# Kernel tuning notes

Measured on AMD Instinct MI355X. Metric: run time of the kernel, lower is better.

Reference implementation:

```python
import jax, jax.numpy as jnp
import numpy as np

VOCAB, HID, KS, VS, EMB = 30, 512, 128, 128, 256
T, N, MAXLEN = 1000, 256, 250

def _lstm_cell(x, h, c, w_ih, w_hh, b_ih, b_hh):
    gates = x @ w_ih.T + h @ w_hh.T + b_ih + b_hh
    i, f, g, o = jnp.split(gates, 4, axis=-1)
    c2 = jax.nn.sigmoid(f) * c + jax.nn.sigmoid(i) * jnp.tanh(g)
    h2 = jax.nn.sigmoid(o) * jnp.tanh(c2)
    return h2, c2

def setup_inputs() -> dict:
    key = jax.random.key(0)
    ks = jax.random.split(key, 20)
    p = lambda k, shp: (jax.random.normal(k, shp, dtype=jnp.float32) * 0.05)
    inp = {
        'keys': jax.random.normal(ks[0], (T, N, KS), dtype=jnp.float32),
        'values': jax.random.normal(ks[1], (T, N, VS), dtype=jnp.float32),
        'seq_lengths': jax.random.randint(ks[2], (N,), 1, T + 1),
        'text': jax.random.randint(ks[3], (N, MAXLEN), 0, VOCAB),
        'embed_W': p(ks[4], (VOCAB, EMB)),
        'w_ih1': p(ks[5], (4 * HID, EMB + VS)), 'w_hh1': p(ks[6], (4 * HID, HID)),
        'b_ih1': jnp.zeros((4 * HID,), jnp.float32), 'b_hh1': jnp.zeros((4 * HID,), jnp.float32),
        'w_ih2': p(ks[7], (4 * HID, HID)), 'w_hh2': p(ks[8], (4 * HID, HID)),
        'b_ih2': jnp.zeros((4 * HID,), jnp.float32), 'b_hh2': jnp.zeros((4 * HID,), jnp.float32),
        'w_ih3': p(ks[9], (4 * KS, HID)), 'w_hh3': p(ks[10], (4 * KS, KS)),
        'b_ih3': jnp.zeros((4 * KS,), jnp.float32), 'b_hh3': jnp.zeros((4 * KS,), jnp.float32),
        'lin_W': p(ks[11], (KS, KS + VS)), 'lin_b': jnp.zeros((KS,), jnp.float32),
        'char_W': p(ks[12], (VOCAB, KS)), 'char_b': jnp.zeros((VOCAB,), jnp.float32),
    }
    return inp

def reference(keys, values, seq_lengths, text, embed_W,
              w_ih1, w_hh1, b_ih1, b_hh1,
              w_ih2, w_hh2, b_ih2, b_hh2,
              w_ih3, w_hh3, b_ih3, b_hh3,
              lin_W, lin_b, char_W, char_b):
    # teacher forcing path (deterministic), dropout is identity in reference
    mask = jnp.arange(T)[None, :] >= seq_lengths[:, None]          # (N, T)
    embs = embed_W[text]                                           # (N, MAXLEN, EMB)
    embs = jnp.swapaxes(embs, 0, 1)                                # (MAXLEN, N, EMB)

    def step(carry, emb_t):
        h1, c1, h2, c2, h3, c3, ctx = carry
        inp1 = jnp.concatenate([emb_t, ctx], axis=1)
        h1, c1 = _lstm_cell(inp1, h1, c1, w_ih1, w_hh1, b_ih1, b_hh1)
        h2, c2 = _lstm_cell(h1, h2, c2, w_ih2, w_hh2, b_ih2, b_hh2)
        h3, c3 = _lstm_cell(h2, h3, c3, w_ih3, w_hh3, b_ih3, b_hh3)
        energy = jnp.einsum('tnk,nk->nt', keys, h3)                # (N, T)
        energy = jnp.where(mask, -1e9, energy)
        attn = jax.nn.softmax(energy, axis=1)
        ctx2 = jnp.einsum('nt,tnv->nv', attn, values)              # (N, VS)
        pred = jnp.concatenate([h3, ctx2], axis=1) @ lin_W.T + lin_b
        pred = pred @ char_W.T + char_b                            # (N, VOCAB)
        return (h1, c1, h2, c2, h3, c3, ctx2), (pred, attn)

    z = lambda d: jnp.zeros((N, d), jnp.float32)
    init = (z(HID), z(HID), z(HID), z(HID), z(KS), z(KS), values[-1])
    _, (preds, attns) = jax.lax.scan(step, init, embs)
    return jnp.swapaxes(preds, 0, 1), attns                        # (N, MAXLEN, VOCAB), (MAXLEN, N, T)
```

## Files before the change

kernel.cpp:

```cpp
#include <hip/hip_runtime.h>

#define VOCAB  30
#define HID    512
#define KS     128
#define VS     128
#define EMB    256
#define TT     1000
#define NB     256
#define MAXLEN 250

#define NH (NB*HID)
#define NK (NB*KS)
#define OFF_CTX (6*NH + 3*NK)
#define WS_TOTAL (OFF_CTX + NK)
#define STATE_BYTES ((size_t)WS_TOTAL * 4)
#define VBF_BYTES   ((size_t)TT * NB * VS * 2)

#define K1 (EMB + VS + HID)
#define K2 (HID + HID)
#define K3 (HID + KS)
#define W1SZ (4*HID*K1)
#define W2SZ (4*HID*K2)
#define W3SZ (4*KS*K3)
#define EMBSZ (VOCAB*EMB)
#define BS1 (4*HID)
#define BS2 (4*HID)
#define BS3 (4*KS)

constexpr size_t NEW_BASE  = STATE_BYTES + VBF_BYTES;
constexpr size_t OFF_W1HI  = NEW_BASE;
constexpr size_t OFF_W1LO  = OFF_W1HI + (size_t)W1SZ*2;
constexpr size_t OFF_W2HI  = OFF_W1LO + (size_t)W1SZ*2;
constexpr size_t OFF_W2LO  = OFF_W2HI + (size_t)W2SZ*2;
constexpr size_t OFF_W3HI  = OFF_W2LO + (size_t)W2SZ*2;
constexpr size_t OFF_W3LO  = OFF_W3HI + (size_t)W3SZ*2;
constexpr size_t OFF_EMBHI = OFF_W3LO + (size_t)W3SZ*2;
constexpr size_t OFF_EMBLO = OFF_EMBHI + (size_t)EMBSZ*2;
constexpr size_t OFF_BSUM  = OFF_EMBLO + (size_t)EMBSZ*2;
constexpr size_t OFF_CTXHI = OFF_BSUM  + (size_t)(BS1+BS2+BS3)*4;
constexpr size_t OFF_CTXLO = OFF_CTXHI + (size_t)NB*VS*2;
constexpr size_t OFF_H1HI  = OFF_CTXLO + (size_t)NB*VS*2;
constexpr size_t OFF_H1LO  = OFF_H1HI + (size_t)2*NH*2;
constexpr size_t OFF_H2HI  = OFF_H1LO + (size_t)2*NH*2;
constexpr size_t OFF_H2LO  = OFF_H2HI + (size_t)2*NH*2;
constexpr size_t OFF_H3HI  = OFF_H2LO + (size_t)2*NH*2;
constexpr size_t OFF_H3LO  = OFF_H3HI + (size_t)2*NK*2;
constexpr size_t OFF_H3F   = OFF_H3LO + (size_t)2*NK*2;
constexpr size_t OFF_C1    = OFF_H3F  + (size_t)NK*4;
constexpr size_t OFF_C2    = OFF_C1 + (size_t)NH*4;
constexpr size_t OFF_C3    = OFF_C2 + (size_t)NH*4;
constexpr size_t FULL_BYTES= OFF_C3 + (size_t)NK*4;
constexpr size_t ZERO_BASE = OFF_H1HI;
constexpr size_t ZERO_BYTES= FULL_BYTES - OFF_H1HI;

typedef __attribute__((ext_vector_type(8))) short bf16x8;
typedef __attribute__((ext_vector_type(4))) float f32x4;
typedef unsigned short u16;

__device__ __forceinline__ float sigmoidf_(float x){ return 1.0f/(1.0f+__expf(-x)); }

__device__ __forceinline__ u16 f2bf_(float x){
    unsigned int u = __float_as_uint(x);
    return (u16)((u + 0x7fffu + ((u >> 16) & 1u)) >> 16);
}
__device__ __forceinline__ float bf2f_(u16 h){ return __uint_as_float((unsigned)h << 16); }


__global__ __launch_bounds__(256)
void pack_w_kernel(const float* __restrict__ wih, const float* __restrict__ whh,
                   u16* __restrict__ hi, u16* __restrict__ lo, int KIN, int KH, int total)
{
    int i = blockIdx.x*256 + threadIdx.x;
    if (i >= total) return;
    const int KW = KIN + KH;
    int g = i / KW, k = i - g*KW;
    float v = (k < KIN) ? wih[g*KIN + k] : whh[g*KH + (k - KIN)];
    u16 h = f2bf_(v);
    hi[i] = h;
    lo[i] = f2bf_(v - bf2f_(h));
}

__global__ __launch_bounds__(256)
void prep_misc_kernel(char* __restrict__ wsb, const float* __restrict__ embW,
                      const float* __restrict__ bi1, const float* __restrict__ bh1,
                      const float* __restrict__ bi2, const float* __restrict__ bh2,
                      const float* __restrict__ bi3, const float* __restrict__ bh3,
                      const float* __restrict__ values)
{
    const int gt = blockIdx.x*256 + threadIdx.x;
    const int gs = gridDim.x*256;
    u16* Ehi = (u16*)(wsb + OFF_EMBHI);
    u16* Elo = (u16*)(wsb + OFF_EMBLO);
    for (int i = gt; i < EMBSZ; i += gs){
        float v = embW[i]; u16 h = f2bf_(v);
        Ehi[i]=h; Elo[i]=f2bf_(v - bf2f_(h));
    }
    float* bs = (float*)(wsb + OFF_BSUM);
    for (int i = gt; i < BS1; i += gs) bs[i]         = bi1[i]+bh1[i];
    for (int i = gt; i < BS2; i += gs) bs[BS1+i]     = bi2[i]+bh2[i];
    for (int i = gt; i < BS3; i += gs) bs[BS1+BS2+i] = bi3[i]+bh3[i];
    u16* Chi = (u16*)(wsb + OFF_CTXHI);
    u16* Clo = (u16*)(wsb + OFF_CTXLO);
    const float* v0 = values + (size_t)(TT-1)*NB*VS;
    for (int i = gt; i < NB*VS; i += gs){
        float v = v0[i]; u16 h = f2bf_(v);
        Chi[i]=h; Clo[i]=f2bf_(v - bf2f_(h));
    }
    uint4* z = (uint4*)(wsb + ZERO_BASE);
    uint4 zz; zz.x=0; zz.y=0; zz.z=0; zz.w=0;
    for (size_t i = (size_t)gt; i < ZERO_BYTES/16; i += (size_t)gs) z[i] = zz;
}


__device__ __forceinline__ void lstm_step(const u16* const wh[4], const u16* const wl[4], int kw,
                                          bf16x8 ah, bf16x8 al, f32x4 acc[4])
{
    #pragma unroll
    for (int q=0;q<4;q++){
        bf16x8 wH = *(const bf16x8*)(wh[q] + kw);
        bf16x8 wL = *(const bf16x8*)(wl[q] + kw);
        acc[q] = __builtin_amdgcn_mfma_f32_16x16x32_bf16(ah, wH, acc[q], 0,0,0);
        acc[q] = __builtin_amdgcn_mfma_f32_16x16x32_bf16(al, wH, acc[q], 0,0,0);
        acc[q] = __builtin_amdgcn_mfma_f32_16x16x32_bf16(ah, wL, acc[q], 0,0,0);
    }
}

template<int H, int KIN, int KH, int MODE>
__global__ __launch_bounds__(128)
void lstm_mfma(const u16* __restrict__ Whi, const u16* __restrict__ Wlo,
               const float* __restrict__ bsum,
               const u16* __restrict__ xhi, const u16* __restrict__ xlo,
               const u16* __restrict__ ehi, const u16* __restrict__ elo,
               const int* __restrict__ text, int step,
               const u16* __restrict__ hphi, const u16* __restrict__ hplo,
               u16* __restrict__ hohi, u16* __restrict__ holo,
               float* __restrict__ hof,
               float* __restrict__ cbuf)
{
    constexpr int KW = KIN + KH;
    constexpr int HT = H/16;
    const int lane = threadIdx.x & 63;
    const int gw   = blockIdx.x*2 + (threadIdx.x >> 6);
    const int ht   = gw % HT, nt = gw / HT;
    const int l15  = lane & 15, lhi = lane >> 4;
    const int n    = nt*16 + l15;
    const int koff = lhi*8;
    const int h0   = ht*16;

    const u16* wh[4]; const u16* wl[4];
    #pragma unroll
    for (int q=0;q<4;q++){
        size_t off = (size_t)(q*H + h0 + l15)*KW + koff;
        wh[q] = Whi + off; wl[q] = Wlo + off;
    }

    f32x4 acc[4];
    f32x4 zr = {0.f,0.f,0.f,0.f};
    #pragma unroll
    for (int q=0;q<4;q++) acc[q] = zr;

    int kb;
    if constexpr (MODE == 0) {
        const int trow = text[n*MAXLEN + step];
        const u16* Eh = ehi + trow*EMB + koff;
        const u16* El = elo + trow*EMB + koff;
        #pragma unroll 4
        for (int s=0;s<EMB/32;s++)
            lstm_step(wh, wl, s*32, *(const bf16x8*)(Eh + s*32), *(const bf16x8*)(El + s*32), acc);
        const u16* Ch = xhi + n*VS + koff;
        const u16* Cl = xlo + n*VS + koff;
        #pragma unroll
        for (int s=0;s<VS/32;s++)
            lstm_step(wh, wl, EMB + s*32, *(const bf16x8*)(Ch + s*32), *(const bf16x8*)(Cl + s*32), acc);
        kb = EMB + VS;
    } else {
        const u16* Xh = xhi + n*KIN + koff;
        const u16* Xl = xlo + n*KIN + koff;
        #pragma unroll 4
        for (int s=0;s<KIN/32;s++)
            lstm_step(wh, wl, s*32, *(const bf16x8*)(Xh + s*32), *(const bf16x8*)(Xl + s*32), acc);
        kb = KIN;
    }
    {
        const u16* Hh = hphi + n*KH + koff;
        const u16* Hl = hplo + n*KH + koff;
        #pragma unroll 4
        for (int s=0;s<KH/32;s++)
            lstm_step(wh, wl, kb + s*32, *(const bf16x8*)(Hh + s*32), *(const bf16x8*)(Hl + s*32), acc);
    }

    const int hcol = h0 + l15;
    const float b0 = bsum[0*H + hcol], b1 = bsum[1*H + hcol];
    const float b2 = bsum[2*H + hcol], b3 = bsum[3*H + hcol];
    const int nr0 = nt*16 + lhi*4;
    #pragma unroll
    for (int r=0;r<4;r++){
        const size_t p = (size_t)(nr0 + r)*H + hcol;
        const float gi = acc[0][r] + b0;
        const float gf = acc[1][r] + b1;
        const float gg = acc[2][r] + b2;
        const float go = acc[3][r] + b3;
        const float cn = sigmoidf_(gf)*cbuf[p] + sigmoidf_(gi)*tanhf(gg);
        const float hn = sigmoidf_(go)*tanhf(cn);
        cbuf[p] = cn;
        const u16 hb = f2bf_(hn);
        hohi[p] = hb;
        holo[p] = f2bf_(hn - bf2f_(hb));
        if (hof) hof[p] = hn;
    }
}


__global__ __launch_bounds__(256)
void init_kernel(float* __restrict__ ws, const float* __restrict__ values){
    int i = blockIdx.x*256 + threadIdx.x;
    if (i >= WS_TOTAL) return;
    if (i < OFF_CTX) ws[i] = 0.0f;
    else ws[i] = values[(size_t)(TT-1)*NB*VS + (i - OFF_CTX)];
}

__global__ __launch_bounds__(256)
void conv_bf16_kernel(const float* __restrict__ src, u16* __restrict__ dst, int n4){
    int i = blockIdx.x*256 + threadIdx.x;
    if (i >= n4) return;
    float4 v = ((const float4*)src)[i];
    ushort4 o;
    o.x = f2bf_(v.x); o.y = f2bf_(v.y); o.z = f2bf_(v.z); o.w = f2bf_(v.w);
    ((ushort4*)dst)[i] = o;
}

template<int H, int KX, int KH, int MODE>
__global__ __launch_bounds__(256)
void lstm_kernel(const float* __restrict__ Wx, const float* __restrict__ Wh,
                 const float* __restrict__ bx, const float* __restrict__ bh,
                 const float* __restrict__ xbuf, const float* __restrict__ embW,
                 const int* __restrict__ text, int step,
                 const float* __restrict__ hread, float* __restrict__ hwrite,
                 float* __restrict__ cbuf)
{
    __shared__ __align__(16) float Xs[16][68];
    __shared__ __align__(16) float Ws[16][68];
    __shared__ float Gs[64][65];

    const int tid = threadIdx.x;
    const int h0  = blockIdx.x * 16;
    const int n0  = blockIdx.y * 64;

    const int sr = tid >> 2;
    const int sk = (tid & 3) << 2;
    const int wrow = (sr >> 4) * H + h0 + (sr & 15);
    const int n  = n0 + sr;

    const int tn4 = (tid & 15) * 4;
    const int tc4 = (tid >> 4) * 4;

    float acc[4][4];
    #pragma unroll
    for (int i=0;i<4;i++){
        #pragma unroll
        for (int j=0;j<4;j++) acc[i][j]=0.0f;
    }

    for (int k0 = 0; k0 < KX + KH; k0 += 16) {
        const int kb = k0 + sk;
        float4 xv, wv;
        if (k0 < KX) {
            if constexpr (MODE == 0) {
                if (kb < EMB) {
                    int idx = text[n * MAXLEN + step];
                    xv = *(const float4*)(embW + idx*EMB + kb);
                } else {
                    xv = *(const float4*)(xbuf + n*VS + (kb - EMB));
                }
            } else {
                xv = *(const float4*)(xbuf + n*KX + kb);
            }
            wv = *(const float4*)(Wx + wrow*KX + kb);
        } else {
            const int kh = kb - KX;
            xv = *(const float4*)(hread + n*KH + kh);
            wv = *(const float4*)(Wh + wrow*KH + kh);
        }
        Xs[sk+0][sr]=xv.x; Xs[sk+1][sr]=xv.y; Xs[sk+2][sr]=xv.z; Xs[sk+3][sr]=xv.w;
        Ws[sk+0][sr]=wv.x; Ws[sk+1][sr]=wv.y; Ws[sk+2][sr]=wv.z; Ws[sk+3][sr]=wv.w;
        __syncthreads();
        #pragma unroll
        for (int kk=0;kk<16;kk++){
            float4 xr = *(const float4*)&Xs[kk][tn4];
            float4 wr = *(const float4*)&Ws[kk][tc4];
            acc[0][0] += wr.x*xr.x; acc[0][1] += wr.x*xr.y; acc[0][2] += wr.x*xr.z; acc[0][3] += wr.x*xr.w;
            acc[1][0] += wr.y*xr.x; acc[1][1] += wr.y*xr.y; acc[1][2] += wr.y*xr.z; acc[1][3] += wr.y*xr.w;
            acc[2][0] += wr.z*xr.x; acc[2][1] += wr.z*xr.y; acc[2][2] += wr.z*xr.z; acc[2][3] += wr.z*xr.w;
            acc[3][0] += wr.w*xr.x; acc[3][1] += wr.w*xr.y; acc[3][2] += wr.w*xr.z; acc[3][3] += wr.w*xr.w;
        }
        __syncthreads();
    }

    #pragma unroll
    for (int ci=0; ci<4; ci++){
        const int c = tc4 + ci;
        const int row = (c >> 4) * H + h0 + (c & 15);
        const float b = bx[row] + bh[row];
        #pragma unroll
        for (int ni=0; ni<4; ni++) Gs[c][tn4+ni] = acc[ci][ni] + b;
    }
    __syncthreads();

    for (int p = tid; p < 16*64; p += 256){
        const int hl = p & 15, nl = p >> 4;
        const float gi = Gs[     hl][nl];
        const float gf = Gs[16 + hl][nl];
        const float gg = Gs[32 + hl][nl];
        const float go = Gs[48 + hl][nl];
        const int gn = n0 + nl, gh = h0 + hl;
        const float cold = cbuf[gn*H + gh];
        const float cn = sigmoidf_(gf)*cold + sigmoidf_(gi)*tanhf(gg);
        const float hn = sigmoidf_(go)*tanhf(cn);
        cbuf[gn*H + gh] = cn;
        hwrite[gn*H + gh] = hn;
    }
}

template<int BF, int CSPLIT>
__global__ __launch_bounds__(512)
void attn_pred_kernel(const float* __restrict__ keys, const void* __restrict__ values_v,
                      const int* __restrict__ seqlen, const float* __restrict__ h3,
                      const float* __restrict__ linW, const float* __restrict__ linb,
                      const float* __restrict__ charW, const float* __restrict__ charb,
                      float* __restrict__ ctx, u16* __restrict__ ctx_hi, u16* __restrict__ ctx_lo,
                      float* __restrict__ out, int step)
{
    __shared__ float es[TT];
    __shared__ float redm[8], reds[8];
    __shared__ float cpart[8][128];
    __shared__ float cat[256];
    __shared__ float mid[128];

    const int tid  = threadIdx.x;
    const int n    = blockIdx.x;
    const int wave = tid >> 6, lane = tid & 63;

    const float2 hv = *(const float2*)(h3 + n*KS + lane*2);
    const int L = seqlen[n];

    for (int t0 = wave*4; t0 < TT; t0 += 32) {
        const float2* kp = (const float2*)(keys + ((size_t)t0*NB + n)*KS) + lane;
        const size_t rs = (size_t)NB*KS/2;
        float2 k0 = kp[0], k1 = kp[rs], k2 = kp[2*rs], k3 = kp[3*rs];
        float d0 = k0.x*hv.x + k0.y*hv.y;
        float d1 = k1.x*hv.x + k1.y*hv.y;
        float d2 = k2.x*hv.x + k2.y*hv.y;
        float d3 = k3.x*hv.x + k3.y*hv.y;
        #pragma unroll
        for (int off=32; off; off>>=1){
            d0 += __shfl_xor(d0, off, 64);
            d1 += __shfl_xor(d1, off, 64);
            d2 += __shfl_xor(d2, off, 64);
            d3 += __shfl_xor(d3, off, 64);
        }
        if (lane == 0){
            es[t0+0] = (t0+0 < L) ? d0 : -1e9f;
            es[t0+1] = (t0+1 < L) ? d1 : -1e9f;
            es[t0+2] = (t0+2 < L) ? d2 : -1e9f;
            es[t0+3] = (t0+3 < L) ? d3 : -1e9f;
        }
    }
    __syncthreads();

    float m = -3e38f;
    for (int t = tid; t < TT; t += 512) m = fmaxf(m, es[t]);
    #pragma unroll
    for (int off=32; off; off>>=1) m = fmaxf(m, __shfl_xor(m, off, 64));
    if (lane == 0) redm[wave] = m;
    __syncthreads();
    m = redm[0];
    #pragma unroll
    for (int w=1; w<8; ++w) m = fmaxf(m, redm[w]);

    float s = 0.0f;
    for (int t = tid; t < TT; t += 512) { float p = __expf(es[t]-m); es[t] = p; s += p; }
    #pragma unroll
    for (int off=32; off; off>>=1) s += __shfl_xor(s, off, 64);
    if (lane == 0) reds[wave] = s;
    __syncthreads();
    s = reds[0];
    #pragma unroll
    for (int w=1; w<8; ++w) s += reds[w];
    const float inv = 1.0f / s;

    float* attn_out = out + (size_t)NB*MAXLEN*VOCAB + ((size_t)step*NB + n)*TT;
    for (int t = tid; t < TT; t += 512) { float a = es[t]*inv; es[t] = a; attn_out[t] = a; }
    __syncthreads();

    float cax = 0.0f, cay = 0.0f;
    if constexpr (BF) {
        const u16* vals = (const u16*)values_v;
        #pragma unroll 4
        for (int j = 0; j < 125; ++j){
            const int t = wave + 8*j;
            const float a = es[t];
            const unsigned int v2 = *((const unsigned int*)(vals + ((size_t)t*NB + n)*VS) + lane);
            cax += a * __uint_as_float(v2 << 16);
            cay += a * __uint_as_float(v2 & 0xffff0000u);
        }
    } else {
        const float* vals = (const float*)values_v;
        #pragma unroll 4
        for (int j = 0; j < 125; ++j){
            const int t = wave + 8*j;
            const float a = es[t];
            const float2 v2 = *((const float2*)(vals + ((size_t)t*NB + n)*VS) + lane);
            cax += a * v2.x;
            cay += a * v2.y;
        }
    }
    cpart[wave][lane*2]   = cax;
    cpart[wave][lane*2+1] = cay;
    __syncthreads();

    if (tid < 128) {
        float cv = 0.0f;
        #pragma unroll
        for (int w=0; w<8; ++w) cv += cpart[w][tid];
        if constexpr (CSPLIT) {
            const u16 hb = f2bf_(cv);
            ctx_hi[n*VS + tid] = hb;
            ctx_lo[n*VS + tid] = f2bf_(cv - bf2f_(hb));
        } else {
            ctx[n*VS + tid] = cv;
        }
        cat[tid]        = h3[n*KS + tid];
        cat[128 + tid]  = cv;
    }
    __syncthreads();

    if (tid < 256) {
        const int o  = tid >> 1;
        const int kh = (tid & 1) * 128;
        const float* w = linW + o*(KS+VS) + kh;
        float a = 0.0f;
        #pragma unroll 8
        for (int k=0; k<128; ++k) a += w[k]*cat[kh+k];
        a += __shfl_xor(a, 1, 64);
        if (!(tid & 1)) mid[o] = a + linb[o];
    }
    __syncthreads();

    if (tid < VOCAB) {
        float a = charb[tid];
        const float* w = charW + tid*KS;
        #pragma unroll 8
        for (int k=0; k<KS; ++k) a += w[k]*mid[k];
        out[((size_t)n*MAXLEN + step)*VOCAB + tid] = a;
    }
}


extern "C" void kernel_launch(void* const* d_in, const int* in_sizes, int n_in,
                              void* d_out, int out_size, void* d_ws, size_t ws_size,
                              hipStream_t stream)
{
    const float* keys   = (const float*)d_in[0];
    const float* values = (const float*)d_in[1];
    const int*   seqlen = (const int*)  d_in[2];
    const int*   text   = (const int*)  d_in[3];
    const float* embW   = (const float*)d_in[4];
    const float* w_ih1  = (const float*)d_in[5];
    const float* w_hh1  = (const float*)d_in[6];
    const float* b_ih1  = (const float*)d_in[7];
    const float* b_hh1  = (const float*)d_in[8];
    const float* w_ih2  = (const float*)d_in[9];
    const float* w_hh2  = (const float*)d_in[10];
    const float* b_ih2  = (const float*)d_in[11];
    const float* b_hh2  = (const float*)d_in[12];
    const float* w_ih3  = (const float*)d_in[13];
    const float* w_hh3  = (const float*)d_in[14];
    const float* b_ih3  = (const float*)d_in[15];
    const float* b_hh3  = (const float*)d_in[16];
    const float* linW   = (const float*)d_in[17];
    const float* linb   = (const float*)d_in[18];
    const float* charW  = (const float*)d_in[19];
    const float* charb  = (const float*)d_in[20];
    float* out = (float*)d_out;
    float* ws  = (float*)d_ws;
    char*  wsb = (char*)d_ws;

    u16* vals_bf = (u16*)(wsb + STATE_BYTES);
    const int n4 = TT*NB*VS/4;

    if (ws_size >= FULL_BYTES) {
        u16* W1hi=(u16*)(wsb+OFF_W1HI); u16* W1lo=(u16*)(wsb+OFF_W1LO);
        u16* W2hi=(u16*)(wsb+OFF_W2HI); u16* W2lo=(u16*)(wsb+OFF_W2LO);
        u16* W3hi=(u16*)(wsb+OFF_W3HI); u16* W3lo=(u16*)(wsb+OFF_W3LO);
        u16* Ehi =(u16*)(wsb+OFF_EMBHI); u16* Elo =(u16*)(wsb+OFF_EMBLO);
        float* bs=(float*)(wsb+OFF_BSUM);
        u16* Chi =(u16*)(wsb+OFF_CTXHI); u16* Clo =(u16*)(wsb+OFF_CTXLO);
        u16* H1hi=(u16*)(wsb+OFF_H1HI);  u16* H1lo=(u16*)(wsb+OFF_H1LO);
        u16* H2hi=(u16*)(wsb+OFF_H2HI);  u16* H2lo=(u16*)(wsb+OFF_H2LO);
        u16* H3hi=(u16*)(wsb+OFF_H3HI);  u16* H3lo=(u16*)(wsb+OFF_H3LO);
        float* H3f=(float*)(wsb+OFF_H3F);
        float* C1=(float*)(wsb+OFF_C1);
        float* C2=(float*)(wsb+OFF_C2);
        float* C3=(float*)(wsb+OFF_C3);

        pack_w_kernel<<<(W1SZ+255)/256, 256, 0, stream>>>(w_ih1, w_hh1, W1hi, W1lo, EMB+VS, HID, W1SZ);
        pack_w_kernel<<<(W2SZ+255)/256, 256, 0, stream>>>(w_ih2, w_hh2, W2hi, W2lo, HID,    HID, W2SZ);
        pack_w_kernel<<<(W3SZ+255)/256, 256, 0, stream>>>(w_ih3, w_hh3, W3hi, W3lo, HID,    KS,  W3SZ);
        conv_bf16_kernel<<<(n4 + 255)/256, 256, 0, stream>>>(values, vals_bf, n4);
        prep_misc_kernel<<<1024, 256, 0, stream>>>(wsb, embW, b_ih1,b_hh1, b_ih2,b_hh2, b_ih3,b_hh3, values);

        constexpr int G12 = (HID/16)*(NB/16)/2;
        constexpr int G3  = (KS/16)*(NB/16)/2;

        for (int t = 0; t < MAXLEN; ++t) {
            const int cur = t & 1, nxt = cur ^ 1;
            lstm_mfma<HID, EMB+VS, HID, 0><<<G12, 128, 0, stream>>>(
                W1hi, W1lo, bs, Chi, Clo, Ehi, Elo, text, t,
                H1hi + cur*NH, H1lo + cur*NH,
                H1hi + nxt*NH, H1lo + nxt*NH, nullptr, C1);
            lstm_mfma<HID, HID, HID, 1><<<G12, 128, 0, stream>>>(
                W2hi, W2lo, bs + BS1, H1hi + nxt*NH, H1lo + nxt*NH, nullptr, nullptr, nullptr, 0,
                H2hi + cur*NH, H2lo + cur*NH,
                H2hi + nxt*NH, H2lo + nxt*NH, nullptr, C2);
            lstm_mfma<KS, HID, KS, 1><<<G3, 128, 0, stream>>>(
                W3hi, W3lo, bs + BS1 + BS2, H2hi + nxt*NH, H2lo + nxt*NH, nullptr, nullptr, nullptr, 0,
                H3hi + cur*NK, H3lo + cur*NK,
                H3hi + nxt*NK, H3lo + nxt*NK, H3f, C3);
            attn_pred_kernel<1,1><<<NB, 512, 0, stream>>>(
                keys, vals_bf, seqlen, H3f, linW, linb, charW, charb,
                nullptr, Chi, Clo, out, t);
        }
        return;
    }

    float* h1  = ws;
    float* c1  = h1 + 2*NH;
    float* h2  = c1 + NH;
    float* c2  = h2 + 2*NH;
    float* h3  = c2 + NH;
    float* c3  = h3 + 2*NK;
    float* ctx = c3 + NK;

    const bool use_bf16 = (ws_size >= STATE_BYTES + VBF_BYTES);

    init_kernel<<<(WS_TOTAL + 255)/256, 256, 0, stream>>>(ws, values);
    if (use_bf16) {
        conv_bf16_kernel<<<(n4 + 255)/256, 256, 0, stream>>>(values, vals_bf, n4);
    }

    for (int t = 0; t < MAXLEN; ++t) {
        const int cur = t & 1, nxt = cur ^ 1;
        lstm_kernel<HID, EMB+VS, HID, 0><<<dim3(HID/16, NB/64), 256, 0, stream>>>(
            w_ih1, w_hh1, b_ih1, b_hh1, ctx, embW, text, t,
            h1 + cur*NH, h1 + nxt*NH, c1);
        lstm_kernel<HID, HID, HID, 1><<<dim3(HID/16, NB/64), 256, 0, stream>>>(
            w_ih2, w_hh2, b_ih2, b_hh2, h1 + nxt*NH, nullptr, nullptr, t,
            h2 + cur*NH, h2 + nxt*NH, c2);
        lstm_kernel<KS, HID, KS, 1><<<dim3(KS/16, NB/64), 256, 0, stream>>>(
            w_ih3, w_hh3, b_ih3, b_hh3, h2 + nxt*NH, nullptr, nullptr, t,
            h3 + cur*NK, h3 + nxt*NK, c3);
        if (use_bf16)
            attn_pred_kernel<1,0><<<NB, 512, 0, stream>>>(
                keys, vals_bf, seqlen, h3 + nxt*NK,
                linW, linb, charW, charb, ctx, nullptr, nullptr, out, t);
        else
            attn_pred_kernel<0,0><<<NB, 512, 0, stream>>>(
                keys, values, seqlen, h3 + nxt*NK,
                linW, linb, charW, charb, ctx, nullptr, nullptr, out, t);
    }
}
```

Before: 33.29 ms.

## Split LSTM gate GEMM K-dimension across four waves with LDS reduction

Each LSTM block now handles one 16x16 output tile with four waves, each covering a quarter of the K dimension, and combines the partial accumulators through shared memory before wave 0 applies the gate nonlinearities. Before, each wave computed a full tile alone. The change quadruples the number of waves per step, which targets the long serial K loop and low occupancy of these small per-timestep launches. Block indices are also remapped so that blocks sharing a weight tile are adjacent, which may help cache locality. The cost is an LDS write/read reduction, a __syncthreads, and three of the four waves sitting idle during the epilogue.

Result: faster. 27.76 ms (-16.6%).

```diff
diff --git a/kernel.cpp b/kernel.cpp
--- a/kernel.cpp
+++ b/kernel.cpp
@@ -126,22 +126,36 @@
 }
 
 template<int H, int KIN, int KH, int MODE>
-__global__ __launch_bounds__(128)
-void lstm_mfma(const u16* __restrict__ Whi, const u16* __restrict__ Wlo,
-               const float* __restrict__ bsum,
-               const u16* __restrict__ xhi, const u16* __restrict__ xlo,
-               const u16* __restrict__ ehi, const u16* __restrict__ elo,
-               const int* __restrict__ text, int step,
-               const u16* __restrict__ hphi, const u16* __restrict__ hplo,
-               u16* __restrict__ hohi, u16* __restrict__ holo,
-               float* __restrict__ hof,
-               float* __restrict__ cbuf)
+__global__ __launch_bounds__(256)
+void lstm_mfma4(const u16* __restrict__ Whi, const u16* __restrict__ Wlo,
+                const float* __restrict__ bsum,
+                const u16* __restrict__ xhi, const u16* __restrict__ xlo,
+                const u16* __restrict__ ehi, const u16* __restrict__ elo,
+                const int* __restrict__ text, int step,
+                const u16* __restrict__ hphi, const u16* __restrict__ hplo,
+                u16* __restrict__ hohi, u16* __restrict__ holo,
+                float* __restrict__ hof,
+                float* __restrict__ cbuf)
 {
-    constexpr int KW = KIN + KH;
-    constexpr int HT = H/16;
-    const int lane = threadIdx.x & 63;
-    const int gw   = blockIdx.x*2 + (threadIdx.x >> 6);
-    const int ht   = gw % HT, nt = gw / HT;
+    constexpr int KW  = KIN + KH;
+    constexpr int HT  = H/16;
+    constexpr int NT  = NB/16;
+    constexpr int S32 = KW/32;
+    constexpr int SPW = S32/4;
+    static_assert(SPW*4 == S32, "K must split 4 ways");
+    static_assert((HT & 7) == 0 || HT == 8, "HT divisible by 8");
+
+    __shared__ float red[3][4][4][64];
+
+    const int tid  = threadIdx.x;
+    const int lane = tid & 63;
+    const int wave = tid >> 6;
+
+    const int bid = blockIdx.x;
+    const int x = bid & 7, j = bid >> 3;
+    const int ht = x*(HT/8) + j/NT;
+    const int nt = j % NT;
+
     const int l15  = lane & 15, lhi = lane >> 4;
     const int n    = nt*16 + l15;
     const int koff = lhi*8;
@@ -159,54 +173,69 @@
     #pragma unroll
     for (int q=0;q<4;q++) acc[q] = zr;
 
-    int kb;
-    if constexpr (MODE == 0) {
+    const u16 *b0h, *b0l;
+    if constexpr (MODE==0){
         const int trow = text[n*MAXLEN + step];
-        const u16* Eh = ehi + trow*EMB + koff;
-        const u16* El = elo + trow*EMB + koff;
-        #pragma unroll 4
-        for (int s=0;s<EMB/32;s++)
-            lstm_step(wh, wl, s*32, *(const bf16x8*)(Eh + s*32), *(const bf16x8*)(El + s*32), acc);
-        const u16* Ch = xhi + n*VS + koff;
-        const u16* Cl = xlo + n*VS + koff;
-        #pragma unroll
-        for (int s=0;s<VS/32;s++)
-            lstm_step(wh, wl, EMB + s*32, *(const bf16x8*)(Ch + s*32), *(const bf16x8*)(Cl + s*32), acc);
-        kb = EMB + VS;
+        b0h = ehi + trow*EMB + koff; b0l = elo + trow*EMB + koff;
     } else {
-        const u16* Xh = xhi + n*KIN + koff;
-        const u16* Xl = xlo + n*KIN + koff;
-        #pragma unroll 4
-        for (int s=0;s<KIN/32;s++)
-            lstm_step(wh, wl, s*32, *(const bf16x8*)(Xh + s*32), *(const bf16x8*)(Xl + s*32), acc);
-        kb = KIN;
-    }
-    {
-        const u16* Hh = hphi + n*KH + koff;
-        const u16* Hl = hplo + n*KH + koff;
-        #pragma unroll 4
-        for (int s=0;s<KH/32;s++)
-            lstm_step(wh, wl, kb + s*32, *(const bf16x8*)(Hh + s*32), *(const bf16x8*)(Hl + s*32), acc);
-    }
-
-    const int hcol = h0 + l15;
-    const float b0 = bsum[0*H + hcol], b1 = bsum[1*H + hcol];
-    const float b2 = bsum[2*H + hcol], b3 = bsum[3*H + hcol];
-    const int nr0 = nt*16 + lhi*4;
-    #pragma unroll
-    for (int r=0;r<4;r++){
-        const size_t p = (size_t)(nr0 + r)*H + hcol;
-        const float gi = acc[0][r] + b0;
-        const float gf = acc[1][r] + b1;
-        const float gg = acc[2][r] + b2;
-        const float go = acc[3][r] + b3;
-        const float cn = sigmoidf_(gf)*cbuf[p] + sigmoidf_(gi)*tanhf(gg);
-        const float hn = sigmoidf_(go)*tanhf(cn);
-        cbuf[p] = cn;
-        const u16 hb = f2bf_(hn);
-        hohi[p] = hb;
-        holo[p] = f2bf_(hn - bf2f_(hb));
-        if (hof) hof[p] = hn;
+        b0h = xhi + n*KIN + koff;    b0l = xlo + n*KIN + koff;
+    }
+    const u16* bch = (MODE==0) ? (xhi + n*VS + koff) : nullptr;
+    const u16* bcl = (MODE==0) ? (xlo + n*VS + koff) : nullptr;
+    const u16* bhh = hphi + n*KH + koff;
+    const u16* bhl = hplo + n*KH + koff;
+
+    #pragma unroll
+    for (int si=0; si<SPW; ++si){
+        const int s = wave*SPW + si;
+        const int k = s*32;
+        const u16 *ph, *pl;
+        if constexpr (MODE==0){
+            if (k < EMB)          { ph = b0h + k;           pl = b0l + k; }
+            else if (k < EMB+VS)  { ph = bch + (k-EMB);     pl = bcl + (k-EMB); }
+            else                  { ph = bhh + (k-EMB-VS);  pl = bhl + (k-EMB-VS); }
+        } else {
+            if (k < KIN)          { ph = b0h + k;           pl = b0l + k; }
+            else                  { ph = bhh + (k-KIN);     pl = bhl + (k-KIN); }
+        }
+        lstm_step(wh, wl, k, *(const bf16x8*)ph, *(const bf16x8*)pl, acc);
+    }
+
+    if (wave >= 1){
+        #pragma unroll
+        for (int q=0;q<4;q++)
+            #pragma unroll
+            for (int r=0;r<4;r++)
+                red[wave-1][q][r][lane] = acc[q][r];
+    }
+    __syncthreads();
+
+    if (wave == 0){
+        #pragma unroll
+        for (int q=0;q<4;q++)
+            #pragma unroll
+            for (int r=0;r<4;r++)
+                acc[q][r] += red[0][q][r][lane] + red[1][q][r][lane] + red[2][q][r][lane];
+
+        const int hcol = h0 + l15;
+        const float bb0 = bsum[0*H + hcol], bb1 = bsum[1*H + hcol];
+        const float bb2 = bsum[2*H + hcol], bb3 = bsum[3*H + hcol];
+        const int nr0 = nt*16 + lhi*4;
+        #pragma unroll
+        for (int r=0;r<4;r++){
+            const size_t p = (size_t)(nr0 + r)*H + hcol;
+            const float gi = acc[0][r] + bb0;
+            const float gf = acc[1][r] + bb1;
+            const float gg = acc[2][r] + bb2;
+            const float go = acc[3][r] + bb3;
+            const float cn = sigmoidf_(gf)*cbuf[p] + sigmoidf_(gi)*tanhf(gg);
+            const float hn = sigmoidf_(go)*tanhf(cn);
+            cbuf[p] = cn;
+            const u16 hb = f2bf_(hn);
+            hohi[p] = hb;
+            holo[p] = f2bf_(hn - bf2f_(hb));
+            if (hof) hof[p] = hn;
+        }
     }
 }
 
@@ -509,20 +538,20 @@
         conv_bf16_kernel<<<(n4 + 255)/256, 256, 0, stream>>>(values, vals_bf, n4);
         prep_misc_kernel<<<1024, 256, 0, stream>>>(wsb, embW, b_ih1,b_hh1, b_ih2,b_hh2, b_ih3,b_hh3, values);
 
-        constexpr int G12 = (HID/16)*(NB/16)/2;
-        constexpr int G3  = (KS/16)*(NB/16)/2;
+        constexpr int G12 = (HID/16)*(NB/16);
+        constexpr int G3  = (KS/16)*(NB/16);
 
         for (int t = 0; t < MAXLEN; ++t) {
             const int cur = t & 1, nxt = cur ^ 1;
-            lstm_mfma<HID, EMB+VS, HID, 0><<<G12, 128, 0, stream>>>(
+            lstm_mfma4<HID, EMB+VS, HID, 0><<<G12, 256, 0, stream>>>(
                 W1hi, W1lo, bs, Chi, Clo, Ehi, Elo, text, t,
                 H1hi + cur*NH, H1lo + cur*NH,
                 H1hi + nxt*NH, H1lo + nxt*NH, nullptr, C1);
-            lstm_mfma<HID, HID, HID, 1><<<G12, 128, 0, stream>>>(
+            lstm_mfma4<HID, HID, HID, 1><<<G12, 256, 0, stream>>>(
                 W2hi, W2lo, bs + BS1, H1hi + nxt*NH, H1lo + nxt*NH, nullptr, nullptr, nullptr, 0,
                 H2hi + cur*NH, H2lo + cur*NH,
                 H2hi + nxt*NH, H2lo + nxt*NH, nullptr, C2);
-            lstm_mfma<KS, HID, KS, 1><<<G3, 128, 0, stream>>>(
+            lstm_mfma4<KS, HID, KS, 1><<<G3, 256, 0, stream>>>(
                 W3hi, W3lo, bs + BS1 + BS2, H2hi + nxt*NH, H2lo + nxt*NH, nullptr, nullptr, nullptr, 0,
                 H3hi + cur*NK, H3lo + cur*NK,
                 H3hi + nxt*NK, H3lo + nxt*NK, H3f, C3);
```
